# Kernel optimization log

Measured on AMD Instinct MI355X. Metric: run time of the kernel, lower is better.

## Reference

```python
import jax, jax.numpy as jnp
import numpy as np

D_MODEL = 64  # per-head dim; temper = sqrt(D_MODEL)
NEG_INF = -1e30  # stand-in for -inf; safe under softmax and autodiff


def setup_inputs() -> dict:
    key = jax.random.key(0)
    kq, kk, kv, km = jax.random.split(key, 4)
    B, S, D = 16, 2048, 64
    q = jax.random.normal(kq, (B, S, D), dtype=jnp.float32)
    k = jax.random.normal(kk, (B, S, D), dtype=jnp.float32)
    v = jax.random.normal(kv, (B, S, D), dtype=jnp.float32)
    attn_mask = jax.random.bernoulli(km, 0.1, (B, S, S))
    return {"q": q, "k": k, "v": v, "attn_mask": attn_mask}


def reference(q, k, v, attn_mask):
    temper = jnp.sqrt(jnp.float32(D_MODEL))
    # [B, Sq, Sk] scores
    attn = jnp.einsum("bqd,bkd->bqk", q, k) / temper
    attn = jnp.where(attn_mask, NEG_INF, attn)
    attn = jax.nn.softmax(attn, axis=2)
    # dropout is identity in eval / attn_dropout=0.0
    output = jnp.einsum("bqk,bkd->bqd", attn, v)
    return (output, attn)
```

## Files before the change

### kernel.cpp

```cpp
#include <hip/hip_runtime.h>
#include <hip/hip_bf16.h>
#include <stdint.h>


#define S_DIM 2048
#define D_DIM 64

typedef short short8 __attribute__((ext_vector_type(8)));
typedef float floatx4 __attribute__((ext_vector_type(4)));
typedef unsigned short ushort4v __attribute__((ext_vector_type(4)));
typedef unsigned short ushort8v __attribute__((ext_vector_type(8)));

__device__ __forceinline__ unsigned short f2bf(float x) {
    uint32_t u = __float_as_uint(x);
    u += 0x7fffu + ((u >> 16) & 1u);
    return (unsigned short)(u >> 16);
}
__device__ __forceinline__ float bf2f(unsigned short h) {
    return __uint_as_float((uint32_t)h << 16);
}

__global__ __launch_bounds__(256) void prep_k(
    const float* __restrict__ k,
    unsigned short* __restrict__ khi, unsigned short* __restrict__ klo)
{
    size_t i = ((size_t)blockIdx.x * 256 + threadIdx.x) * 4;
    float4 x = *(const float4*)(k + i);
    float xs[4] = {x.x, x.y, x.z, x.w};
    ushort4v h, l;
    #pragma unroll
    for (int p = 0; p < 4; ++p) {
        unsigned short hp = f2bf(xs[p]);
        h[p] = hp;
        l[p] = f2bf(xs[p] - bf2f(hp));
    }
    *(ushort4v*)(khi + i) = h;
    *(ushort4v*)(klo + i) = l;
}

__global__ __launch_bounds__(256) void prep_v(
    const float* __restrict__ v, unsigned short* __restrict__ vt)
{
    __shared__ unsigned short tile[64][66];
    const int b  = blockIdx.x >> 5;
    const int s0 = (blockIdx.x & 31) * 64;
    #pragma unroll
    for (int i = 0; i < 4; ++i) {
        int e = threadIdx.x + i * 256;
        int key = e >> 4, d4 = (e & 15) * 4;
        float4 x = *(const float4*)(v + ((size_t)(b * S_DIM + s0 + key)) * D_DIM + d4);
        tile[key][d4 + 0] = f2bf(x.x);
        tile[key][d4 + 1] = f2bf(x.y);
        tile[key][d4 + 2] = f2bf(x.z);
        tile[key][d4 + 3] = f2bf(x.w);
    }
    __syncthreads();
    const int d  = threadIdx.x >> 2;
    const int k0 = (threadIdx.x & 3) * 16;
    union { unsigned short u[16]; ushort8v v8[2]; } T;
    #pragma unroll
    for (int j = 0; j < 16; ++j) T.u[j] = tile[k0 + j][d];
    unsigned short* dst = vt + ((size_t)(b * D_DIM + d)) * S_DIM + s0 + k0;
    *(ushort8v*)dst       = T.v8[0];
    *(ushort8v*)(dst + 8) = T.v8[1];
}

__global__ __launch_bounds__(512) void attn_fused_v2b(
    const float* __restrict__ q,
    const unsigned short* __restrict__ khi, const unsigned short* __restrict__ klo,
    const unsigned short* __restrict__ vt,
    const int* __restrict__ mask,
    float* __restrict__ out, float* __restrict__ attn)
{
    __shared__ __align__(16) float qlds[16 * 68];
    __shared__ __align__(16) unsigned short pbuf[8 * 16 * 36];
    __shared__ __align__(16) float obuf[8 * 16 * 68];
    __shared__ float mxtab[8 * 16];
    __shared__ float ltab[8 * 16];

    const int tid  = threadIdx.x;
    const int w    = tid >> 6;
    const int lane = tid & 63;
    const int quad = lane >> 4;
    const int n16  = lane & 15;
    const int b    = blockIdx.x >> 7;
    const int q0   = (blockIdx.x & 127) * 16;
    const int key0 = w * 256;

    {
        int m = tid >> 5, d = (tid & 31) * 2;
        float2 qv = *(const float2*)(q + ((size_t)(b * S_DIM + q0 + m)) * D_DIM + d);
        qlds[m * 68 + d]     = qv.x;
        qlds[m * 68 + d + 1] = qv.y;
    }
    __syncthreads();

    short8 ahi[2], alo[2];
    #pragma unroll
    for (int s = 0; s < 2; ++s) {
        const float* qp = &qlds[n16 * 68 + s * 32 + quad * 8];
        union { unsigned short u[8]; short8 v; } H, L;
        #pragma unroll
        for (int p = 0; p < 8; ++p) {
            float x = qp[p];
            unsigned short hp = f2bf(x);
            H.u[p] = hp;
            L.u[p] = f2bf(x - bf2f(hp));
        }
        ahi[s] = H.v; alo[s] = L.v;
    }

    floatx4 sc[16];
    const unsigned short* khb = khi + (size_t)(b * S_DIM) * D_DIM;
    const unsigned short* klb = klo + (size_t)(b * S_DIM) * D_DIM;
    #pragma unroll
    for (int c = 0; c < 16; ++c) {
        const int key = key0 + c * 16 + n16;
        const int* mp = mask + (size_t)(b * S_DIM + q0 + quad * 4) * S_DIM + key;
        int mk0 = mp[0], mk1 = mp[S_DIM], mk2 = mp[2 * S_DIM], mk3 = mp[3 * S_DIM];
        floatx4 acc = {0.f, 0.f, 0.f, 0.f};
        #pragma unroll
        for (int s = 0; s < 2; ++s) {
            const size_t off = (size_t)key * D_DIM + s * 32 + quad * 8;
            short8 BH = *(const short8*)(khb + off);
            short8 BL = *(const short8*)(klb + off);
            acc = __builtin_amdgcn_mfma_f32_16x16x32_bf16(ahi[s], BH, acc, 0, 0, 0);
            acc = __builtin_amdgcn_mfma_f32_16x16x32_bf16(ahi[s], BL, acc, 0, 0, 0);
            acc = __builtin_amdgcn_mfma_f32_16x16x32_bf16(alo[s], BH, acc, 0, 0, 0);
        }
        sc[c][0] = mk0 ? -1e30f : acc[0] * 0.125f;
        sc[c][1] = mk1 ? -1e30f : acc[1] * 0.125f;
        sc[c][2] = mk2 ? -1e30f : acc[2] * 0.125f;
        sc[c][3] = mk3 ? -1e30f : acc[3] * 0.125f;
    }

    #pragma unroll
    for (int r = 0; r < 4; ++r) {
        float mx = sc[0][r];
        #pragma unroll
        for (int c = 1; c < 16; ++c) mx = fmaxf(mx, sc[c][r]);
        #pragma unroll
        for (int o = 1; o < 16; o <<= 1) mx = fmaxf(mx, __shfl_xor(mx, o, 64));
        if (n16 == 0) mxtab[w * 16 + quad * 4 + r] = mx;
    }
    __syncthreads();
    #pragma unroll
    for (int r = 0; r < 4; ++r) {
        float mf = -3e38f;
        #pragma unroll
        for (int w2 = 0; w2 < 8; ++w2) mf = fmaxf(mf, mxtab[w2 * 16 + quad * 4 + r]);
        float l = 0.f;
        #pragma unroll
        for (int c = 0; c < 16; ++c) {
            float e = __expf(sc[c][r] - mf);
            sc[c][r] = e;
            l += e;
        }
        #pragma unroll
        for (int o = 1; o < 16; o <<= 1) l += __shfl_xor(l, o, 64);
        if (n16 == 0) ltab[w * 16 + quad * 4 + r] = l;
    }
    __syncthreads();
    #pragma unroll
    for (int r = 0; r < 4; ++r) {
        float l = 0.f;
        #pragma unroll
        for (int w2 = 0; w2 < 8; ++w2) l += ltab[w2 * 16 + quad * 4 + r];
        float inv = 1.0f / l;
        #pragma unroll
        for (int c = 0; c < 16; ++c) sc[c][r] *= inv;
    }

    {
        float* arow = attn + (size_t)(b * S_DIM + q0 + quad * 4) * S_DIM + key0 + n16;
        #pragma unroll
        for (int c = 0; c < 16; ++c) {
            #pragma unroll
            for (int r = 0; r < 4; ++r) arow[(size_t)r * S_DIM + c * 16] = sc[c][r];
        }
    }

    floatx4 o0 = {0,0,0,0}, o1 = {0,0,0,0}, o2 = {0,0,0,0}, o3 = {0,0,0,0};
    unsigned short* pw = pbuf + w * 576;
    const unsigned short* vtb = vt + (size_t)b * D_DIM * S_DIM;
    #pragma unroll
    for (int s2 = 0; s2 < 8; ++s2) {
        #pragma unroll
        for (int h = 0; h < 2; ++h) {
            const int c = s2 * 2 + h;
            #pragma unroll
            for (int r = 0; r < 4; ++r)
                pw[(quad * 4 + r) * 36 + h * 16 + n16] = f2bf(sc[c][r]);
        }
        __syncthreads();
        short8 pa;
        {
            const uint32_t* pr = (const uint32_t*)((const char*)pbuf +
                                   (size_t)w * 1152 + n16 * 72 + quad * 16);
            union { uint32_t u[4]; short8 v; } P;
            P.u[0] = pr[0]; P.u[1] = pr[1]; P.u[2] = pr[2]; P.u[3] = pr[3];
            pa = P.v;
        }
        const int keyb = key0 + s2 * 32 + quad * 8;
        #pragma unroll
        for (int nc = 0; nc < 4; ++nc) {
            short8 bv = *(const short8*)(vtb + (size_t)(nc * 16 + n16) * S_DIM + keyb);
            floatx4& oo = (nc == 0 ? o0 : nc == 1 ? o1 : nc == 2 ? o2 : o3);
            oo = __builtin_amdgcn_mfma_f32_16x16x32_bf16(pa, bv, oo, 0, 0, 0);
        }
        __syncthreads();
    }

    #pragma unroll
    for (int nc = 0; nc < 4; ++nc) {
        floatx4 oo = (nc == 0 ? o0 : nc == 1 ? o1 : nc == 2 ? o2 : o3);
        #pragma unroll
        for (int i = 0; i < 4; ++i)
            obuf[(w * 16 + quad * 4 + i) * 68 + nc * 16 + n16] = oo[i];
    }
    __syncthreads();
    #pragma unroll
    for (int t2 = 0; t2 < 2; ++t2) {
        int idx = tid + t2 * 512;
        int m = idx >> 6, d = idx & 63;
        float a = 0.f;
        #pragma unroll
        for (int w2 = 0; w2 < 8; ++w2) a += obuf[(w2 * 16 + m) * 68 + d];
        out[(size_t)(b * S_DIM + q0 + m) * D_DIM + d] = a;
    }
}

__global__ __launch_bounds__(512) void attn_fused_v1(
    const float* __restrict__ q, const float* __restrict__ k,
    const float* __restrict__ v, const int* __restrict__ mask,
    float* __restrict__ out, float* __restrict__ attn)
{
    __shared__ __align__(16) float qlds[16 * 68];
    __shared__ __align__(16) unsigned short pbuf[8 * 16 * 36];
    __shared__ __align__(16) float obuf[8 * 16 * 68];
    __shared__ float mxtab[8 * 16];
    __shared__ float ltab[8 * 16];

    const int tid  = threadIdx.x;
    const int w    = tid >> 6;
    const int lane = tid & 63;
    const int quad = lane >> 4;
    const int n16  = lane & 15;
    const int b    = blockIdx.x >> 7;
    const int q0   = (blockIdx.x & 127) * 16;
    const int key0 = w * 256;

    {
        int m = tid >> 5, d = (tid & 31) * 2;
        float2 qv = *(const float2*)(q + ((size_t)(b * S_DIM + q0 + m)) * D_DIM + d);
        qlds[m * 68 + d]     = qv.x;
        qlds[m * 68 + d + 1] = qv.y;
    }
    __syncthreads();

    short8 ahi[2], alo[2];
    #pragma unroll
    for (int s = 0; s < 2; ++s) {
        const float* qp = &qlds[n16 * 68 + s * 32 + quad * 8];
        union { __hip_bfloat162 h[4]; short8 v; } H, L;
        #pragma unroll
        for (int p = 0; p < 4; ++p) {
            float x0 = qp[2 * p], x1 = qp[2 * p + 1];
            __hip_bfloat162 h2 = __float22bfloat162_rn(float2{x0, x1});
            float l0 = x0 - __bfloat162float(h2.x);
            float l1 = x1 - __bfloat162float(h2.y);
            H.h[p] = h2;
            L.h[p] = __float22bfloat162_rn(float2{l0, l1});
        }
        ahi[s] = H.v; alo[s] = L.v;
    }

    floatx4 sc[16];
    const size_t kvbase = (size_t)(b * S_DIM) * D_DIM;
    #pragma unroll
    for (int c = 0; c < 16; ++c) {
        const int key = key0 + c * 16 + n16;
        const int* mp = mask + (size_t)(b * S_DIM + q0 + quad * 4) * S_DIM + key;
        int mk0 = mp[0], mk1 = mp[S_DIM], mk2 = mp[2 * S_DIM], mk3 = mp[3 * S_DIM];
        floatx4 acc = {0.f, 0.f, 0.f, 0.f};
        #pragma unroll
        for (int s = 0; s < 2; ++s) {
            const float* kp = k + kvbase + (size_t)key * D_DIM + s * 32 + quad * 8;
            float4 k0 = *(const float4*)kp;
            float4 k1 = *(const float4*)(kp + 4);
            float kf[8] = {k0.x, k0.y, k0.z, k0.w, k1.x, k1.y, k1.z, k1.w};
            union { __hip_bfloat162 h[4]; short8 v; } BH, BL;
            #pragma unroll
            for (int p = 0; p < 4; ++p) {
                float x0 = kf[2 * p], x1 = kf[2 * p + 1];
                __hip_bfloat162 h2 = __float22bfloat162_rn(float2{x0, x1});
                BH.h[p] = h2;
                BL.h[p] = __float22bfloat162_rn(
                    float2{x0 - __bfloat162float(h2.x), x1 - __bfloat162float(h2.y)});
            }
            acc = __builtin_amdgcn_mfma_f32_16x16x32_bf16(ahi[s], BH.v, acc, 0, 0, 0);
            acc = __builtin_amdgcn_mfma_f32_16x16x32_bf16(ahi[s], BL.v, acc, 0, 0, 0);
            acc = __builtin_amdgcn_mfma_f32_16x16x32_bf16(alo[s], BH.v, acc, 0, 0, 0);
        }
        sc[c][0] = mk0 ? -1e30f : acc[0] * 0.125f;
        sc[c][1] = mk1 ? -1e30f : acc[1] * 0.125f;
        sc[c][2] = mk2 ? -1e30f : acc[2] * 0.125f;
        sc[c][3] = mk3 ? -1e30f : acc[3] * 0.125f;
    }

    #pragma unroll
    for (int r = 0; r < 4; ++r) {
        float mx = sc[0][r];
        #pragma unroll
        for (int c = 1; c < 16; ++c) mx = fmaxf(mx, sc[c][r]);
        #pragma unroll
        for (int o = 1; o < 16; o <<= 1) mx = fmaxf(mx, __shfl_xor(mx, o, 64));
        if (n16 == 0) mxtab[w * 16 + quad * 4 + r] = mx;
    }
    __syncthreads();
    #pragma unroll
    for (int r = 0; r < 4; ++r) {
        float mf = -3e38f;
        #pragma unroll
        for (int w2 = 0; w2 < 8; ++w2) mf = fmaxf(mf, mxtab[w2 * 16 + quad * 4 + r]);
        float l = 0.f;
        #pragma unroll
        for (int c = 0; c < 16; ++c) {
            float e = __expf(sc[c][r] - mf);
            sc[c][r] = e;
            l += e;
        }
        #pragma unroll
        for (int o = 1; o < 16; o <<= 1) l += __shfl_xor(l, o, 64);
        if (n16 == 0) ltab[w * 16 + quad * 4 + r] = l;
    }
    __syncthreads();
    #pragma unroll
    for (int r = 0; r < 4; ++r) {
        float l = 0.f;
        #pragma unroll
        for (int w2 = 0; w2 < 8; ++w2) l += ltab[w2 * 16 + quad * 4 + r];
        float inv = 1.0f / l;
        #pragma unroll
        for (int c = 0; c < 16; ++c) sc[c][r] *= inv;
    }

    {
        float* arow = attn + (size_t)(b * S_DIM + q0 + quad * 4) * S_DIM + key0 + n16;
        #pragma unroll
        for (int c = 0; c < 16; ++c) {
            #pragma unroll
            for (int r = 0; r < 4; ++r) arow[(size_t)r * S_DIM + c * 16] = sc[c][r];
        }
    }

    floatx4 o0 = {0,0,0,0}, o1 = {0,0,0,0}, o2 = {0,0,0,0}, o3 = {0,0,0,0};
    unsigned short* pw = pbuf + w * 576;
    #pragma unroll
    for (int s2 = 0; s2 < 8; ++s2) {
        #pragma unroll
        for (int h = 0; h < 2; ++h) {
            const int c = s2 * 2 + h;
            #pragma unroll
            for (int r = 0; r < 4; ++r)
                pw[(quad * 4 + r) * 36 + h * 16 + n16] = f2bf(sc[c][r]);
        }
        __syncthreads();
        short8 pa;
        {
            const uint32_t* pr = (const uint32_t*)((const char*)pbuf +
                                   (size_t)w * 1152 + n16 * 72 + quad * 16);
            union { uint32_t u[4]; short8 v; } P;
            P.u[0] = pr[0]; P.u[1] = pr[1]; P.u[2] = pr[2]; P.u[3] = pr[3];
            pa = P.v;
        }
        const size_t vrow0 = (size_t)(b * S_DIM + key0 + s2 * 32 + quad * 8) * D_DIM;
        #pragma unroll
        for (int nc = 0; nc < 4; ++nc) {
            const float* vp = v + vrow0 + nc * 16 + n16;
            union { __hip_bfloat162 h[4]; short8 v8; } BV;
            #pragma unroll
            for (int p = 0; p < 4; ++p) {
                float x0 = vp[(size_t)(2 * p) * D_DIM];
                float x1 = vp[(size_t)(2 * p + 1) * D_DIM];
                BV.h[p] = __float22bfloat162_rn(float2{x0, x1});
            }
            floatx4& oo = (nc == 0 ? o0 : nc == 1 ? o1 : nc == 2 ? o2 : o3);
            oo = __builtin_amdgcn_mfma_f32_16x16x32_bf16(pa, BV.v8, oo, 0, 0, 0);
        }
        __syncthreads();
    }

    #pragma unroll
    for (int nc = 0; nc < 4; ++nc) {
        floatx4 oo = (nc == 0 ? o0 : nc == 1 ? o1 : nc == 2 ? o2 : o3);
        #pragma unroll
        for (int i = 0; i < 4; ++i)
            obuf[(w * 16 + quad * 4 + i) * 68 + nc * 16 + n16] = oo[i];
    }
    __syncthreads();
    #pragma unroll
    for (int t2 = 0; t2 < 2; ++t2) {
        int idx = tid + t2 * 512;
        int m = idx >> 6, d = idx & 63;
        float a = 0.f;
        #pragma unroll
        for (int w2 = 0; w2 < 8; ++w2) a += obuf[(w2 * 16 + m) * 68 + d];
        out[(size_t)(b * S_DIM + q0 + m) * D_DIM + d] = a;
    }
}

extern "C" void kernel_launch(void* const* d_in, const int* in_sizes, int n_in,
                              void* d_out, int out_size, void* d_ws, size_t ws_size,
                              hipStream_t stream) {
    const float* q    = (const float*)d_in[0];
    const float* k    = (const float*)d_in[1];
    const float* v    = (const float*)d_in[2];
    const int*   mask = (const int*)d_in[3];

    float* out  = (float*)d_out;
    float* attn = out + (size_t)16 * S_DIM * D_DIM;

    const size_t NE = (size_t)16 * S_DIM * D_DIM;
    if (d_ws != nullptr && ws_size >= NE * 2 * 3) {
        unsigned short* khi = (unsigned short*)d_ws;
        unsigned short* klo = khi + NE;
        unsigned short* vtp = klo + NE;
        prep_k<<<dim3(2048), dim3(256), 0, stream>>>(k, khi, klo);
        prep_v<<<dim3(512),  dim3(256), 0, stream>>>(v, vtp);
        attn_fused_v2b<<<dim3(2048), dim3(512), 0, stream>>>(q, khi, klo, vtp, mask, out, attn);
    } else {
        attn_fused_v1<<<dim3(2048), dim3(512), 0, stream>>>(q, k, v, mask, out, attn);
    }
}
```

Before: 641.4 us.

## Pre-swizzle K/V into MFMA fragment layout and bit-pack the mask

```diff
diff --git a/kernel.cpp b/kernel.cpp
--- a/kernel.cpp
+++ b/kernel.cpp
@@ -8,8 +8,8 @@
 
 typedef short short8 __attribute__((ext_vector_type(8)));
 typedef float floatx4 __attribute__((ext_vector_type(4)));
-typedef unsigned short ushort4v __attribute__((ext_vector_type(4)));
 typedef unsigned short ushort8v __attribute__((ext_vector_type(8)));
+typedef uint32_t u32a __attribute__((may_alias));
 
 __device__ __forceinline__ unsigned short f2bf(float x) {
     uint32_t u = __float_as_uint(x);
@@ -20,56 +20,62 @@
     return __uint_as_float((uint32_t)h << 16);
 }
 
-__global__ __launch_bounds__(256) void prep_k(
+__global__ __launch_bounds__(256) void prep_mask(
+    const int* __restrict__ mask, uint32_t* __restrict__ bits)
+{
+    size_t i = (size_t)blockIdx.x * 256 + threadIdx.x;
+    int m = mask[i];
+    unsigned long long bal = __ballot(m != 0);
+    int lane = threadIdx.x & 63;
+    if ((lane & 31) == 0)
+        bits[i >> 5] = (uint32_t)(bal >> ((lane >> 5) * 32));
+}
+
+__global__ __launch_bounds__(128) void prep_k2(
     const float* __restrict__ k,
-    unsigned short* __restrict__ khi, unsigned short* __restrict__ klo)
+    unsigned short* __restrict__ khi2, unsigned short* __restrict__ klo2)
 {
-    size_t i = ((size_t)blockIdx.x * 256 + threadIdx.x) * 4;
-    float4 x = *(const float4*)(k + i);
-    float xs[4] = {x.x, x.y, x.z, x.w};
-    ushort4v h, l;
-    #pragma unroll
-    for (int p = 0; p < 4; ++p) {
-        unsigned short hp = f2bf(xs[p]);
-        h[p] = hp;
-        l[p] = f2bf(xs[p] - bf2f(hp));
-    }
-    *(ushort4v*)(khi + i) = h;
-    *(ushort4v*)(klo + i) = l;
-}
-
-__global__ __launch_bounds__(256) void prep_v(
-    const float* __restrict__ v, unsigned short* __restrict__ vt)
+    const int b  = blockIdx.x >> 7;
+    const int kc = blockIdx.x & 127;
+    const int t  = threadIdx.x;
+    const int s = t >> 6, quad = (t >> 4) & 3, n16 = t & 15;
+    const float* src = k + ((size_t)(b * S_DIM) + kc * 16 + n16) * D_DIM + s * 32 + quad * 8;
+    float4 x0 = *(const float4*)src;
+    float4 x1 = *(const float4*)(src + 4);
+    float xs[8] = {x0.x, x0.y, x0.z, x0.w, x1.x, x1.y, x1.z, x1.w};
+    ushort8v h, l;
+    #pragma unroll
+    for (int e = 0; e < 8; ++e) {
+        unsigned short hp = f2bf(xs[e]);
+        h[e] = hp;
+        l[e] = f2bf(xs[e] - bf2f(hp));
+    }
+    size_t o = ((size_t)(b * 128 + kc)) * 1024 + (size_t)t * 8;
+    *(ushort8v*)(khi2 + o) = h;
+    *(ushort8v*)(klo2 + o) = l;
+}
+
+__global__ __launch_bounds__(256) void prep_v2(
+    const float* __restrict__ v, unsigned short* __restrict__ vfrag)
 {
-    __shared__ unsigned short tile[64][66];
-    const int b  = blockIdx.x >> 5;
-    const int s0 = (blockIdx.x & 31) * 64;
-    #pragma unroll
-    for (int i = 0; i < 4; ++i) {
-        int e = threadIdx.x + i * 256;
-        int key = e >> 4, d4 = (e & 15) * 4;
-        float4 x = *(const float4*)(v + ((size_t)(b * S_DIM + s0 + key)) * D_DIM + d4);
-        tile[key][d4 + 0] = f2bf(x.x);
-        tile[key][d4 + 1] = f2bf(x.y);
-        tile[key][d4 + 2] = f2bf(x.z);
-        tile[key][d4 + 3] = f2bf(x.w);
-    }
-    __syncthreads();
-    const int d  = threadIdx.x >> 2;
-    const int k0 = (threadIdx.x & 3) * 16;
-    union { unsigned short u[16]; ushort8v v8[2]; } T;
-    #pragma unroll
-    for (int j = 0; j < 16; ++j) T.u[j] = tile[k0 + j][d];
-    unsigned short* dst = vt + ((size_t)(b * D_DIM + d)) * S_DIM + s0 + k0;
-    *(ushort8v*)dst       = T.v8[0];
-    *(ushort8v*)(dst + 8) = T.v8[1];
-}
-
-__global__ __launch_bounds__(512) void attn_fused_v2b(
+    const int b  = blockIdx.x >> 6;
+    const int kb = blockIdx.x & 63;
+    const int t  = threadIdx.x;
+    const int nc = t >> 6, quad = (t >> 4) & 3, n16 = t & 15;
+    ushort8v o;
+    #pragma unroll
+    for (int e = 0; e < 8; ++e) {
+        float x = v[((size_t)(b * S_DIM) + kb * 32 + quad * 8 + e) * D_DIM + nc * 16 + n16];
+        o[e] = f2bf(x);
+    }
+    *(ushort8v*)(vfrag + ((size_t)(b * 64 + kb)) * 2048 + (size_t)t * 8) = o;
+}
+
+__global__ __launch_bounds__(512) void attn_fused_v3(
     const float* __restrict__ q,
-    const unsigned short* __restrict__ khi, const unsigned short* __restrict__ klo,
-    const unsigned short* __restrict__ vt,
-    const int* __restrict__ mask,
+    const unsigned short* __restrict__ khi2, const unsigned short* __restrict__ klo2,
+    const unsigned short* __restrict__ vfrag,
+    const uint32_t* __restrict__ bits,
     float* __restrict__ out, float* __restrict__ attn)
 {
     __shared__ __align__(16) float qlds[16 * 68];
@@ -87,6 +93,14 @@
     const int q0   = (blockIdx.x & 127) * 16;
     const int key0 = w * 256;
 
+    uint32_t blo, bhi;
+    {
+        const uint32_t* bsrc = bits +
+            ((size_t)(b * S_DIM) + q0 + (lane >> 2)) * 64 + w * 8 + 2 * (lane & 3);
+        uint2 bt = *(const uint2*)bsrc;
+        blo = bt.x; bhi = bt.y;
+    }
+
     {
         int m = tid >> 5, d = (tid & 31) * 2;
         float2 qv = *(const float2*)(q + ((size_t)(b * S_DIM + q0 + m)) * D_DIM + d);
@@ -111,27 +125,32 @@
     }
 
     floatx4 sc[16];
-    const unsigned short* khb = khi + (size_t)(b * S_DIM) * D_DIM;
-    const unsigned short* klb = klo + (size_t)(b * S_DIM) * D_DIM;
+    const unsigned short* khb = khi2 + (size_t)b * 131072;
+    const unsigned short* klb = klo2 + (size_t)b * 131072;
     #pragma unroll
     for (int c = 0; c < 16; ++c) {
-        const int key = key0 + c * 16 + n16;
-        const int* mp = mask + (size_t)(b * S_DIM + q0 + quad * 4) * S_DIM + key;
-        int mk0 = mp[0], mk1 = mp[S_DIM], mk2 = mp[2 * S_DIM], mk3 = mp[3 * S_DIM];
+        const int kc = w * 16 + c;
         floatx4 acc = {0.f, 0.f, 0.f, 0.f};
         #pragma unroll
         for (int s = 0; s < 2; ++s) {
-            const size_t off = (size_t)key * D_DIM + s * 32 + quad * 8;
+            const size_t off = (size_t)((kc * 2 + s) * 4 + quad) * 128 + n16 * 8;
             short8 BH = *(const short8*)(khb + off);
             short8 BL = *(const short8*)(klb + off);
             acc = __builtin_amdgcn_mfma_f32_16x16x32_bf16(ahi[s], BH, acc, 0, 0, 0);
             acc = __builtin_amdgcn_mfma_f32_16x16x32_bf16(ahi[s], BL, acc, 0, 0, 0);
             acc = __builtin_amdgcn_mfma_f32_16x16x32_bf16(alo[s], BH, acc, 0, 0, 0);
         }
-        sc[c][0] = mk0 ? -1e30f : acc[0] * 0.125f;
-        sc[c][1] = mk1 ? -1e30f : acc[1] * 0.125f;
-        sc[c][2] = mk2 ? -1e30f : acc[2] * 0.125f;
-        sc[c][3] = mk3 ? -1e30f : acc[3] * 0.125f;
+        sc[c] = acc;
+    }
+    #pragma unroll
+    for (int r = 0; r < 4; ++r) {
+        #pragma unroll
+        for (int c = 0; c < 16; ++c) {
+            int srcl = quad * 16 + r * 4 + (c >> 2);
+            uint32_t d = (uint32_t)__shfl((int)((c & 2) ? bhi : blo), srcl, 64);
+            uint32_t bit = (d >> ((c & 1) * 16 + n16)) & 1u;
+            sc[c][r] = bit ? -1e30f : sc[c][r] * 0.125f;
+        }
     }
 
     #pragma unroll
@@ -182,7 +201,7 @@
 
     floatx4 o0 = {0,0,0,0}, o1 = {0,0,0,0}, o2 = {0,0,0,0}, o3 = {0,0,0,0};
     unsigned short* pw = pbuf + w * 576;
-    const unsigned short* vtb = vt + (size_t)b * D_DIM * S_DIM;
+    const unsigned short* vtb = vfrag + (size_t)b * 131072;
     #pragma unroll
     for (int s2 = 0; s2 < 8; ++s2) {
         #pragma unroll
@@ -192,23 +211,22 @@
             for (int r = 0; r < 4; ++r)
                 pw[(quad * 4 + r) * 36 + h * 16 + n16] = f2bf(sc[c][r]);
         }
-        __syncthreads();
         short8 pa;
         {
-            const uint32_t* pr = (const uint32_t*)((const char*)pbuf +
+            const u32a* pr = (const u32a*)((const char*)pbuf +
                                    (size_t)w * 1152 + n16 * 72 + quad * 16);
             union { uint32_t u[4]; short8 v; } P;
             P.u[0] = pr[0]; P.u[1] = pr[1]; P.u[2] = pr[2]; P.u[3] = pr[3];
             pa = P.v;
         }
-        const int keyb = key0 + s2 * 32 + quad * 8;
+        const int kb = w * 8 + s2;
         #pragma unroll
         for (int nc = 0; nc < 4; ++nc) {
-            short8 bv = *(const short8*)(vtb + (size_t)(nc * 16 + n16) * S_DIM + keyb);
+            const size_t off = (size_t)((kb * 4 + nc) * 4 + quad) * 128 + n16 * 8;
+            short8 bv = *(const short8*)(vtb + off);
             floatx4& oo = (nc == 0 ? o0 : nc == 1 ? o1 : nc == 2 ? o2 : o3);
             oo = __builtin_amdgcn_mfma_f32_16x16x32_bf16(pa, bv, oo, 0, 0, 0);
         }
-        __syncthreads();
     }
 
     #pragma unroll
@@ -422,13 +440,16 @@
     float* attn = out + (size_t)16 * S_DIM * D_DIM;
 
     const size_t NE = (size_t)16 * S_DIM * D_DIM;
-    if (d_ws != nullptr && ws_size >= NE * 2 * 3) {
-        unsigned short* khi = (unsigned short*)d_ws;
-        unsigned short* klo = khi + NE;
-        unsigned short* vtp = klo + NE;
-        prep_k<<<dim3(2048), dim3(256), 0, stream>>>(k, khi, klo);
-        prep_v<<<dim3(512),  dim3(256), 0, stream>>>(v, vtp);
-        attn_fused_v2b<<<dim3(2048), dim3(512), 0, stream>>>(q, khi, klo, vtp, mask, out, attn);
+    const size_t need = NE * 2 * 3 + NE * 4;
+    if (d_ws != nullptr && ws_size >= need) {
+        unsigned short* khi2  = (unsigned short*)d_ws;
+        unsigned short* klo2  = khi2 + NE;
+        unsigned short* vfrag = klo2 + NE;
+        uint32_t*       bits  = (uint32_t*)(vfrag + NE);
+        prep_mask<<<dim3(262144), dim3(256), 0, stream>>>(mask, bits);
+        prep_k2<<<dim3(2048), dim3(128), 0, stream>>>(k, khi2, klo2);
+        prep_v2<<<dim3(1024), dim3(256), 0, stream>>>(v, vfrag);
+        attn_fused_v3<<<dim3(2048), dim3(512), 0, stream>>>(q, khi2, klo2, vfrag, bits, out, attn);
     } else {
         attn_fused_v1<<<dim3(2048), dim3(512), 0, stream>>>(q, k, v, mask, out, attn);
     }
```

New measurement: 634.8 us. Within noise of the previous version (-1.0%).
